# Performance work log

Measured on AMD Instinct MI355X. Metric: run time of the kernel, lower is better.

## Reference

```python
import jax, jax.numpy as jnp
import numpy as np

N_NODE = 200000   # item catalog size (n_node)
EMB = 100         # emb_size
NNZ = 1000000     # hypergraph adjacency nonzeros
B = 1024          # batch / cl_size
L = 50            # session length
LAYERS = 2        # HyperConv layers (opt.layer)
TAU = 0.2         # contrastive temperature
K_NEI = 3         # FindNeighbors.neighbor_n


def setup_inputs() -> dict:
    key = jax.random.key(0)
    ks = jax.random.split(key, 16)
    g = 1.414 / np.sqrt(EMB)  # xavier_normal gain=1.414 scale
    inp = {}
    inp["embedding"] = jax.random.normal(ks[0], (N_NODE, EMB), jnp.float32) * 0.1
    inp["adj_val"] = jax.random.uniform(ks[1], (NNZ,), jnp.float32)
    inp["A"] = jax.random.uniform(ks[2], (B, B), jnp.float32) * 0.01
    inp["D"] = jax.random.uniform(ks[3], (B, B), jnp.float32) * 0.01
    inp["z2"] = jax.random.normal(ks[4], (B, EMB), jnp.float32)
    inp["Wcf1"] = jax.random.normal(ks[5], (EMB, EMB), jnp.float32) * g
    inp["bcf1"] = jnp.zeros((EMB,), jnp.float32)
    inp["Wcf2"] = jax.random.normal(ks[6], (EMB, EMB), jnp.float32) * g
    inp["bcf2"] = jnp.zeros((EMB,), jnp.float32)
    inp["Wkg1"] = jax.random.normal(ks[7], (EMB, EMB), jnp.float32) * g
    inp["bkg1"] = jnp.zeros((EMB,), jnp.float32)
    inp["Wkg2"] = jax.random.normal(ks[8], (EMB, EMB), jnp.float32) * g
    inp["bkg2"] = jnp.zeros((EMB,), jnp.float32)
    inp["session_len"] = jnp.full((B, 1), float(L), jnp.float32)
    inp["adj_row"] = jax.random.randint(ks[9], (NNZ,), 0, N_NODE, jnp.int32)
    inp["adj_col"] = jax.random.randint(ks[10], (NNZ,), 0, N_NODE, jnp.int32)
    inp["items"] = jax.random.randint(ks[11], (B, L), 0, N_NODE + 1, jnp.int32)
    return inp


def _proj(z, W1, b1, W2, b2):
    # nn.Linear -> ELU -> nn.Linear (Contrast_2view projector)
    return jax.nn.elu(z @ W1.T + b1) @ W2.T + b2


def reference(embedding, adj_val, A, D, z2,
              Wcf1, bcf1, Wcf2, bcf2, Wkg1, bkg1, Wkg2, bkg2,
              session_len, adj_row, adj_col, items):
    # ---- HyperConv: layered sparse propagation, averaged over layers ----
    h = embedding
    acc = embedding
    for _ in range(LAYERS):
        # torch.sparse.mm(adjacency, h) via gather + segment_sum
        h = jax.ops.segment_sum(adj_val[:, None] * h[adj_col], adj_row,
                                num_segments=N_NODE)
        acc = acc + h
    hyper = acc / (LAYERS + 1)  # [N_NODE, EMB]

    # ---- RelationGAT.forward ----
    emb_pad = jnp.concatenate([jnp.zeros((1, EMB), hyper.dtype), hyper], axis=0)
    seq_h = emb_pad[items]                       # [B, L, EMB]
    rel = jnp.sum(seq_h, axis=1) / session_len   # [B, EMB]
    rel = (D @ A) @ rel                          # session-graph conv
    c = jax.nn.selu(rel)
    l_c = c / jnp.linalg.norm(c, axis=-1, keepdims=True)  # [B, EMB]

    # ---- FindNeighbors (dropout omitted: eval mode) ----
    sess = l_c
    norms = jnp.sqrt(jnp.sum(sess * sess + 1e-6, axis=1, keepdims=True))
    cos = (sess @ sess.T) / (norms @ norms.T)    # [B, B]
    cos = jax.nn.softmax(cos, axis=-1)
    topv, topi = jax.lax.top_k(cos, K_NEI)       # [B, K]
    topv = jax.nn.softmax(topv, axis=-1)
    neighbor = jnp.sum(topv[:, :, None] * sess[topi], axis=1)  # [B, EMB]

    # ---- Contrast_2view ----
    z1p = _proj(sess, Wcf1, bcf1, Wcf2, bcf2)
    z2p = _proj(z2, Wkg1, bkg1, Wkg2, bkg2)
    n1 = jnp.linalg.norm(z1p, axis=-1, keepdims=True)
    n2 = jnp.linalg.norm(z2p, axis=-1, keepdims=True)
    simm = jnp.exp((z1p @ z2p.T) / (n1 @ n2.T) / TAU)
    simm = simm / (jnp.sum(simm, axis=1, keepdims=True) + 1e-8)
    cl_loss = -jnp.mean(jnp.log(jnp.diagonal(simm)))  # pos = eye

    return hyper, l_c, neighbor, cl_loss
```

## Files before the change

### kernel.cpp

```cpp
#include <hip/hip_runtime.h>
#include <hip/hip_bf16.h>

#define N_NODE 200000
#define EMB 100
#define NNZ 1000000
#define BATCH 1024
#define SLEN 50
#define BE (BATCH * EMB)
#define SCAN_BLK 1024
#define PROJ_ROWS 8
#define UNR 8
#define HIST_BLOCKS 977

#define OFF_LC    20000000LL
#define OFF_NB    20102400LL
#define OFF_LOSS  20204800LL

typedef __hip_bfloat16 bf16;

__device__ __forceinline__ float b2f(bf16 x) { return __bfloat162float(x); }
__device__ __forceinline__ bf16 f2b(float x) { return __float2bfloat16(x); }

__device__ __forceinline__ float ldf(const void* p, long long i, int f32) {
    return f32 ? ((const float*)p)[i] : b2f(((const bf16*)p)[i]);
}
__device__ __forceinline__ void stf(void* p, long long i, int f32, float v) {
    if (f32) ((float*)p)[i] = v;
    else     ((bf16*)p)[i] = f2b(v);
}

__device__ __forceinline__ float bfb2f(unsigned short s) {
    return __uint_as_float(((unsigned)s) << 16);
}
__device__ __forceinline__ unsigned short f2bfb(float x) {
    bf16 h = f2b(x); unsigned short r; __builtin_memcpy(&r, &h, 2); return r;
}
__device__ __forceinline__ float2 up2(unsigned u) {
    return make_float2(bfb2f((unsigned short)(u & 0xffff)), bfb2f((unsigned short)(u >> 16)));
}
__device__ __forceinline__ unsigned pk2(float a, float b) {
    return (unsigned)f2bfb(a) | ((unsigned)f2bfb(b) << 16);
}
__device__ __forceinline__ float2 ldf2(const void* p, long long pi, int f32) {
    if (f32) return ((const float2*)p)[pi];
    return up2(((const unsigned*)p)[pi]);
}
template<bool F32>
__device__ __forceinline__ float2 ldf2t(const void* p, long long pi) {
    if (F32) return ((const float2*)p)[pi];
    return up2(((const unsigned*)p)[pi]);
}
template<bool F32>
__device__ __forceinline__ float2 ldnt2(const void* p, long long pi) {
    if (F32) {
        unsigned long long u = __builtin_nontemporal_load((const unsigned long long*)p + pi);
        return make_float2(__uint_as_float((unsigned)u), __uint_as_float((unsigned)(u >> 32)));
    }
    return up2(__builtin_nontemporal_load((const unsigned*)p + pi));
}
__device__ __forceinline__ float2 ldnt_h1(const unsigned* p, long long pi) {
    return up2(__builtin_nontemporal_load(p + pi));
}
__device__ __forceinline__ void stf2(void* p, long long pi, int f32, float a, float b) {
    if (f32) ((float2*)p)[pi] = make_float2(a, b);
    else     ((unsigned*)p)[pi] = pk2(a, b);
}

__device__ __forceinline__ float wave_allreduce_sum(float v) {
    for (int m = 32; m > 0; m >>= 1) v += __shfl_xor(v, m, 64);
    return v;
}

__global__ void hist_repack(const int* __restrict__ rows, int* __restrict__ counts,
                            const void* __restrict__ adjval, int* __restrict__ flag,
                            const void* __restrict__ emb, void* __restrict__ embp,
                            int f32h) {
    if (blockIdx.x == 0 && threadIdx.x == 0) {
        int f = 0;
        const bf16* p = (const bf16*)adjval;
        for (int i = 0; i < 64; i++) {
            float x = b2f(p[i]);
            if (!(x >= 0.0f && x <= 1.0f)) f = 1;
        }
        *flag = f;
    }
    if (blockIdx.x < HIST_BLOCKS) {
        int e0 = (blockIdx.x * 256 + threadIdx.x) * 4;
        if (e0 < NNZ) {
            int4 r4 = *(const int4*)&rows[e0];
            atomicAdd(&counts[r4.x], 1);
            atomicAdd(&counts[r4.y], 1);
            atomicAdd(&counts[r4.z], 1);
            atomicAdd(&counts[r4.w], 1);
        }
        return;
    }
    long long idx = (long long)(blockIdx.x - HIST_BLOCKS) * 256 + threadIdx.x;
    if (idx >= (long long)N_NODE * 64) return;
    long long r = idx >> 6;
    int l = (int)(idx & 63);
    float2 v = make_float2(0.f, 0.f);
    if (l < 50) v = ldf2(emb, r * 50 + l, f32h);
    stf2(embp, r * 64 + l, f32h, v.x, v.y);
}

__global__ void scan_block(const int* __restrict__ counts, int* __restrict__ incl,
                           int* __restrict__ bsums) {
    __shared__ int s[SCAN_BLK];
    int i = blockIdx.x * SCAN_BLK + threadIdx.x;
    int v = (i < N_NODE) ? counts[i] : 0;
    s[threadIdx.x] = v;
    __syncthreads();
    for (int off = 1; off < SCAN_BLK; off <<= 1) {
        int add = (threadIdx.x >= (unsigned)off) ? s[threadIdx.x - off] : 0;
        __syncthreads();
        s[threadIdx.x] += add;
        __syncthreads();
    }
    if (i < N_NODE) incl[i] = s[threadIdx.x];
    if (threadIdx.x == SCAN_BLK - 1) bsums[blockIdx.x] = s[threadIdx.x];
}

__global__ void scan_add(const int* __restrict__ counts, const int* __restrict__ incl,
                         const int* __restrict__ bsums, int* __restrict__ row_ptr,
                         int* __restrict__ cursor, int nb) {
    __shared__ int s[256];
    int t = threadIdx.x;
    if (t < 256) s[t] = (t < nb) ? bsums[t] : 0;
    __syncthreads();
    for (int off = 1; off < 256; off <<= 1) {
        int add = 0;
        if (t < 256 && t >= off) add = s[t - off];
        __syncthreads();
        if (t < 256) s[t] += add;
        __syncthreads();
    }
    int base = (blockIdx.x == 0) ? 0 : s[blockIdx.x - 1];
    int i = blockIdx.x * SCAN_BLK + t;
    if (i < N_NODE) {
        int ex = incl[i] - counts[i] + base;
        row_ptr[i] = ex;
        cursor[i] = ex;
    }
    if (i == 0) row_ptr[N_NODE] = NNZ;
}

__global__ void permute_edges(const int* __restrict__ arow, const int* __restrict__ acol,
                              const void* __restrict__ aval, int* __restrict__ cursor,
                              int2* __restrict__ cv, const int* __restrict__ flagp) {
    const int f32 = *flagp;
    if (blockIdx.x == 0 && threadIdx.x < 8) cv[NNZ + threadIdx.x] = make_int2(0, 0);
    int e0 = (blockIdx.x * 256 + threadIdx.x) * 4;
    if (e0 >= NNZ) return;
    int4 r4 = *(const int4*)&arow[e0];
    int4 c4 = *(const int4*)&acol[e0];
    float v[4];
    if (f32) {
        float4 f = *(const float4*)((const float*)aval + e0);
        v[0] = f.x; v[1] = f.y; v[2] = f.z; v[3] = f.w;
    } else {
        const unsigned* p = (const unsigned*)aval;
        unsigned u0 = p[e0 >> 1], u1 = p[(e0 >> 1) + 1];
        float2 a = up2(u0), b = up2(u1);
        v[0] = a.x; v[1] = a.y; v[2] = b.x; v[3] = b.y;
    }
    int rr[4] = {r4.x, r4.y, r4.z, r4.w};
    int cc[4] = {c4.x, c4.y, c4.z, c4.w};
    #pragma unroll
    for (int j = 0; j < 4; j++) {
        int pos = atomicAdd(&cursor[rr[j]], 1);
        cv[pos] = make_int2(cc[j], __float_as_int(v[j]));
    }
}

__device__ __forceinline__ void ld_cv8(int2* c, const int2* __restrict__ cv, int k0) {
    #pragma unroll
    for (int j = 0; j < UNR; j++) c[j] = cv[k0 + j];
}

template<bool F32>
__device__ __forceinline__ void spmm1_body(
        const int* __restrict__ rp, const int2* __restrict__ cv,
        const void* __restrict__ src, int estride, unsigned* __restrict__ h1) {
    int lane = threadIdx.x & 63;
    int r = blockIdx.x * 4 + (threadIdx.x >> 6);
    if (r >= N_NODE) return;
    bool act = lane < 50;
    int pl = (estride == 64) ? lane : (act ? lane : 0);
    int k0 = rp[r], k1 = rp[r + 1];
    int2 c[UNR];
    ld_cv8(c, cv, k0);
    int c0x = c[0].x;
    float2 e[UNR];
    #pragma unroll
    for (int j = 0; j < UNR; j++) {
        int cl = (k0 + j < k1) ? c[j].x : c0x;
        e[j] = ldnt2<F32>(src, (long long)cl * estride + pl);
    }
    float a0 = 0.f, a1 = 0.f;
    #pragma unroll
    for (int j = 0; j < UNR; j++) {
        float v = (k0 + j < k1) ? __int_as_float(c[j].y) : 0.f;
        a0 += v * e[j].x; a1 += v * e[j].y;
    }
    for (int k = k0 + UNR; k < k1; k += UNR) {
        int2 ct[UNR];
        #pragma unroll
        for (int j = 0; j < UNR; j++) { int kk = k + j; ct[j] = cv[kk < k1 ? kk : k1 - 1]; }
        float2 et[UNR];
        #pragma unroll
        for (int j = 0; j < UNR; j++)
            et[j] = ldnt2<F32>(src, (long long)ct[j].x * estride + pl);
        #pragma unroll
        for (int j = 0; j < UNR; j++) {
            float v = (k + j < k1) ? __int_as_float(ct[j].y) : 0.f;
            a0 += v * et[j].x; a1 += v * et[j].y;
        }
    }
    h1[(long long)r * 64 + lane] = pk2(a0, a1);
}

__global__ __launch_bounds__(256) void spmm_gather1(
        const int* __restrict__ rp, const int2* __restrict__ cv,
        const void* __restrict__ src, int estride,
        unsigned* __restrict__ h1, const int* __restrict__ flagp) {
    if (*flagp) spmm1_body<true>(rp, cv, src, estride, h1);
    else        spmm1_body<false>(rp, cv, src, estride, h1);
}

template<bool F32>
__device__ __forceinline__ void spmm2_body(
        const int* __restrict__ rp, const int2* __restrict__ cv,
        const void* __restrict__ emb,
        const unsigned* __restrict__ h1, void* __restrict__ out) {
    int lane = threadIdx.x & 63;
    int r = blockIdx.x * 4 + (threadIdx.x >> 6);
    if (r >= N_NODE) return;
    bool act = lane < 50;
    int pl = act ? lane : 0;
    int k0 = rp[r], k1 = rp[r + 1];
    int2 c[UNR];
    ld_cv8(c, cv, k0);
    int c0x = c[0].x;
    float2 ebv = ldf2t<F32>(emb, (long long)r * 50 + pl);
    float2 h1r = up2(h1[(long long)r * 64 + lane]);
    float2 e[UNR];
    #pragma unroll
    for (int j = 0; j < UNR; j++) {
        int cl = (k0 + j < k1) ? c[j].x : c0x;
        e[j] = ldnt_h1(h1, (long long)cl * 64 + lane);
    }
    float a0 = 0.f, a1 = 0.f;
    #pragma unroll
    for (int j = 0; j < UNR; j++) {
        float v = (k0 + j < k1) ? __int_as_float(c[j].y) : 0.f;
        a0 += v * e[j].x; a1 += v * e[j].y;
    }
    for (int k = k0 + UNR; k < k1; k += UNR) {
        int2 ct[UNR];
        #pragma unroll
        for (int j = 0; j < UNR; j++) { int kk = k + j; ct[j] = cv[kk < k1 ? kk : k1 - 1]; }
        float2 et[UNR];
        #pragma unroll
        for (int j = 0; j < UNR; j++)
            et[j] = ldnt_h1(h1, (long long)ct[j].x * 64 + lane);
        #pragma unroll
        for (int j = 0; j < UNR; j++) {
            float v = (k + j < k1) ? __int_as_float(ct[j].y) : 0.f;
            a0 += v * et[j].x; a1 += v * et[j].y;
        }
    }
    if (act)
        stf2(out, (long long)r * 50 + lane, F32 ? 1 : 0,
             (ebv.x + h1r.x + a0) * (1.0f / 3.0f), (ebv.y + h1r.y + a1) * (1.0f / 3.0f));
}

__global__ __launch_bounds__(256) void spmm_gather2(
        const int* __restrict__ rp, const int2* __restrict__ cv,
        const void* __restrict__ emb,
        const unsigned* __restrict__ h1, void* __restrict__ out,
        const int* __restrict__ flagp) {
    if (*flagp) spmm2_body<true>(rp, cv, emb, h1, out);
    else        spmm2_body<false>(rp, cv, emb, h1, out);
}

template<bool F32>
__device__ __forceinline__ void rel_rows_body(
        const void* __restrict__ out, const int* __restrict__ items,
        const void* __restrict__ slen, float* __restrict__ rel) {
    int lane = threadIdx.x & 63;
    int b = blockIdx.x * 4 + (threadIdx.x >> 6);
    if (b >= BATCH || lane >= 50) return;
    float s0 = 0.f, s1 = 0.f;
    #pragma unroll
    for (int l0 = 0; l0 < SLEN; l0 += 10) {
        int it[10];
        #pragma unroll
        for (int j = 0; j < 10; j++) it[j] = items[b * SLEN + l0 + j];
        float2 e[10];
        #pragma unroll
        for (int j = 0; j < 10; j++) {
            int idx = (it[j] > 0) ? it[j] - 1 : 0;
            e[j] = ldf2t<F32>(out, (long long)idx * 50 + lane);
        }
        #pragma unroll
        for (int j = 0; j < 10; j++) {
            float m = (it[j] > 0) ? 1.f : 0.f;
            s0 += m * e[j].x; s1 += m * e[j].y;
        }
    }
    float inv = 1.0f / ldf(slen, b, F32 ? 1 : 0);
    ((float2*)rel)[b * 50 + lane] = make_float2(s0 * inv, s1 * inv);
}

__global__ __launch_bounds__(256) void rel_rows(
        const void* __restrict__ out, const int* __restrict__ items,
        const void* __restrict__ slen, float* __restrict__ rel,
        const int* __restrict__ flagp) {
    if (*flagp) rel_rows_body<true>(out, items, slen, rel);
    else        rel_rows_body<false>(out, items, slen, rel);
}

__device__ __forceinline__ void bmm0_dev(float* smem, const void* __restrict__ M,
                                         const float* __restrict__ X, float* __restrict__ Y,
                                         int f32, int blk) {
    float (*ms)[BATCH] = (float(*)[BATCH])smem;
    int i0 = blk * 4;
    int t = threadIdx.x;
    for (int idx = t; idx < 4 * BATCH; idx += 256) {
        int rr = idx >> 10, j = idx & 1023;
        ms[rr][j] = ldf(M, (long long)(i0 + rr) * BATCH + j, f32);
    }
    __syncthreads();
    int w = t >> 6, lane = t & 63;
    if (lane >= 50) return;
    int i = i0 + w;
    const float2* X2 = (const float2*)X;
    float s0 = 0.f, s1 = 0.f;
    for (int j = 0; j < BATCH; j++) {
        float m = ms[w][j];
        float2 x = X2[j * 50 + lane];
        s0 += m * x.x; s1 += m * x.y;
    }
    ((float2*)Y)[i * 50 + lane] = make_float2(s0, s1);
}

__device__ void proj_dev(float* smem, const void* __restrict__ X, int x_dual,
                         const void* __restrict__ W1, const void* __restrict__ B1,
                         const void* __restrict__ W2, const void* __restrict__ B2,
                         float* __restrict__ Z, float* __restrict__ ZT,
                         float* __restrict__ nrm, int f32, int blk) {
    float* wT = smem;
    float* bsh = smem + 10000;
    float (*hid)[EMB] = (float(*)[EMB])(smem + 10100);
    float (*xr)[EMB]  = (float(*)[EMB])(smem + 10900);
    float (*red2)[2]  = (float(*)[2])(smem + 11100);
    int t = threadIdx.x;
    int sub = t >> 7, u = t & 127;
    int r0 = blk * PROJ_ROWS;
    for (int idx = t; idx < EMB * EMB; idx += 256) {
        int o = idx / EMB, k = idx - o * EMB;
        wT[k * EMB + o] = ldf(W1, idx, f32);
    }
    if (t < EMB) bsh[t] = ldf(B1, t, f32);
    __syncthreads();
    for (int pr = 0; pr < PROJ_ROWS; pr += 2) {
        int row = r0 + pr + sub;
        if (u < EMB)
            xr[sub][u] = x_dual ? ldf(X, (long long)row * EMB + u, f32)
                                : ((const float*)X)[row * EMB + u];
        __syncthreads();
        if (u < EMB) {
            float s = bsh[u];
            for (int k = 0; k < EMB; k++) s += xr[sub][k] * wT[k * EMB + u];
            hid[pr + sub][u] = (s > 0.f) ? s : expm1f(s);
        }
        __syncthreads();
    }
    for (int idx = t; idx < EMB * EMB; idx += 256) {
        int o = idx / EMB, k = idx - o * EMB;
        wT[k * EMB + o] = ldf(W2, idx, f32);
    }
    if (t < EMB) bsh[t] = ldf(B2, t, f32);
    __syncthreads();
    for (int pr = 0; pr < PROJ_ROWS; pr += 2) {
        int row = r0 + pr + sub;
        float sq = 0.f;
        if (u < EMB) {
            float o = bsh[u];
            const float* h = hid[pr + sub];
            for (int k = 0; k < EMB; k++) o += h[k] * wT[k * EMB + u];
            Z[(long long)row * EMB + u] = o;
            if (ZT) ZT[(long long)u * BATCH + row] = o;
            sq = o * o;
        }
        sq = wave_allreduce_sum(sq);
        if ((t & 63) == 0) red2[sub][(t >> 6) & 1] = sq;
        __syncthreads();
        if (u == 0) nrm[row] = sqrtf(red2[sub][0] + red2[sub][1]);
        __syncthreads();
    }
}

__global__ __launch_bounds__(256) void bmm1_projz2(
        const void* __restrict__ A, const float* __restrict__ relv, float* __restrict__ t1,
        const void* __restrict__ z2,
        const void* __restrict__ W1, const void* __restrict__ B1,
        const void* __restrict__ W2, const void* __restrict__ B2,
        float* __restrict__ z2p, float* __restrict__ z2pT, float* __restrict__ n2,
        const int* __restrict__ flagp) {
    __shared__ float smem[11104];
    const int f32 = *flagp;
    if (blockIdx.x < 256) bmm0_dev(smem, A, relv, t1, f32, blockIdx.x);
    else proj_dev(smem, z2, 1, W1, B1, W2, B2, z2p, z2pT, n2, f32, blockIdx.x - 256);
}

__global__ __launch_bounds__(256) void bmm2_selu(const void* __restrict__ M,
                                                 const float* __restrict__ X,
                                                 float* __restrict__ sess,
                                                 float* __restrict__ sessT,
                                                 float* __restrict__ ns,
                                                 void* __restrict__ out,
                                                 float* __restrict__ lacc,
                                                 int* __restrict__ done,
                                                 const int* __restrict__ flagp) {
    __shared__ float ms[4][BATCH];
    const int f32 = *flagp;
    if (blockIdx.x == 0 && threadIdx.x == 0) { *lacc = 0.f; *done = 0; }
    int i0 = blockIdx.x * 4;
    int t = threadIdx.x;
    for (int idx = t; idx < 4 * BATCH; idx += 256) {
        int rr = idx >> 10, j = idx & 1023;
        ms[rr][j] = ldf(M, (long long)(i0 + rr) * BATCH + j, f32);
    }
    __syncthreads();
    int w = t >> 6, lane = t & 63;
    bool act = lane < 50;
    int i = i0 + w;
    float s0 = 0.f, s1 = 0.f;
    if (act) {
        const float2* X2 = (const float2*)X;
        for (int j = 0; j < BATCH; j++) {
            float m = ms[w][j];
            float2 x = X2[j * 50 + lane];
            s0 += m * x.x; s1 += m * x.y;
        }
    }
    const float sc = 1.0507009873554804934193349852946f;
    const float al = 1.6732632423543772848170429916717f;
    float c0 = (s0 > 0.f) ? sc * s0 : sc * (al * expm1f(s0));
    float c1 = (s1 > 0.f) ? sc * s1 : sc * (al * expm1f(s1));
    if (!act) { c0 = 0.f; c1 = 0.f; }
    float nrm = sqrtf(wave_allreduce_sum(c0 * c0 + c1 * c1));
    float l0 = c0 / nrm, l1 = c1 / nrm;
    float nterm = act ? (l0 * l0 + l1 * l1 + 2e-6f) : 0.f;
    float n2sum = wave_allreduce_sum(nterm);
    if (act) {
        ((float2*)sess)[i * 50 + lane] = make_float2(l0, l1);
        sessT[(2 * lane) * BATCH + i] = l0;
        sessT[(2 * lane + 1) * BATCH + i] = l1;
        stf2(out, OFF_LC / 2 + (long long)i * 50 + lane, f32, l0, l1);
    }
    if (lane == 0) ns[i] = sqrtf(n2sum);
}

__device__ void neighbor_dev(float* smem, const float* __restrict__ sess,
                             const float* __restrict__ sessT, const float* __restrict__ ns,
                             void* __restrict__ out, int f32, int i) {
    float* si  = smem;
    float* red = smem + 100;
    float* wrv = smem + 104;
    int*   wri = (int*)(smem + 108);
    float* chv = smem + 112;
    int*   chi = (int*)(smem + 115);
    float* stv = smem + 118;
    int t = threadIdx.x;
    if (t < EMB) si[t] = sess[i * EMB + t];
    __syncthreads();
    float ni = ns[i];
    float d0 = 0.f, d1 = 0.f, d2 = 0.f, d3 = 0.f;
    for (int k = 0; k < EMB; k++) {
        float sv = si[k];
        const float* row = sessT + k * BATCH;
        d0 += sv * row[t];
        d1 += sv * row[t + 256];
        d2 += sv * row[t + 512];
        d3 += sv * row[t + 768];
    }
    float pv0 = expf(d0 / (ni * ns[t]));
    float pv1 = expf(d1 / (ni * ns[t + 256]));
    float pv2 = expf(d2 / (ni * ns[t + 512]));
    float pv3 = expf(d3 / (ni * ns[t + 768]));
    float local = pv0 + pv1 + pv2 + pv3;
    float w = wave_allreduce_sum(local);
    if ((t & 63) == 0) red[t >> 6] = w;
    __syncthreads();
    float S = red[0] + red[1] + red[2] + red[3];

    int c0 = -1, c1 = -1, c2 = -1;
    float pv[4] = {pv0, pv1, pv2, pv3};
    for (int r = 0; r < 3; r++) {
        float bv = -1e30f; int bi = 0x7fffffff;
        #pragma unroll
        for (int m = 0; m < 4; m++) {
            int j = t + (m << 8);
            if (j == c0 || j == c1 || j == c2) continue;
            float v = pv[m];
            if (v > bv || (v == bv && j < bi)) { bv = v; bi = j; }
        }
        #pragma unroll
        for (int off = 1; off < 64; off <<= 1) {
            float ov = __shfl_xor(bv, off);
            int oi = __shfl_xor(bi, off);
            if (ov > bv || (ov == bv && oi < bi)) { bv = ov; bi = oi; }
        }
        if ((t & 63) == 0) { wrv[t >> 6] = bv; wri[t >> 6] = bi; }
        __syncthreads();
        if (t == 0) {
            float fv = wrv[0]; int fi = wri[0];
            for (int wq = 1; wq < 4; wq++) {
                if (wrv[wq] > fv || (wrv[wq] == fv && wri[wq] < fi)) { fv = wrv[wq]; fi = wri[wq]; }
            }
            chv[r] = fv; chi[r] = fi;
        }
        __syncthreads();
        if (r == 0) c0 = chi[0];
        else if (r == 1) c1 = chi[1];
        else c2 = chi[2];
    }
    if (t == 0) {
        float e0 = expf(chv[0] / S), e1 = expf(chv[1] / S), e2 = expf(chv[2] / S);
        float es = e0 + e1 + e2;
        stv[0] = e0 / es; stv[1] = e1 / es; stv[2] = e2 / es;
    }
    __syncthreads();
    if (t < EMB) {
        float o = stv[0] * sess[chi[0] * EMB + t]
                + stv[1] * sess[chi[1] * EMB + t]
                + stv[2] * sess[chi[2] * EMB + t];
        stf(out, OFF_NB + i * EMB + t, f32, o);
    }
}

__global__ __launch_bounds__(256) void neighbor_projz1(
        const float* __restrict__ sess, const float* __restrict__ sessT,
        const float* __restrict__ ns, void* __restrict__ out,
        const void* __restrict__ W1, const void* __restrict__ B1,
        const void* __restrict__ W2, const void* __restrict__ B2,
        float* __restrict__ z1p, float* __restrict__ n1,
        const int* __restrict__ flagp) {
    __shared__ float smem[11104];
    const int f32 = *flagp;
    if (blockIdx.x < BATCH) neighbor_dev(smem, sess, sessT, ns, out, f32, blockIdx.x);
    else proj_dev(smem, sess, 0, W1, B1, W2, B2, z1p, nullptr, n1, f32,
                  blockIdx.x - BATCH);
}

__global__ void loss_kernel(const float* __restrict__ z1p, const float* __restrict__ z2pT,
                            const float* __restrict__ n1, const float* __restrict__ n2,
                            float* __restrict__ acc, int* __restrict__ done,
                            void* __restrict__ out, const int* __restrict__ flagp) {
    __shared__ float zi[EMB];
    __shared__ float red[4];
    __shared__ float sdiag;
    const int f32 = *flagp;
    int i = blockIdx.x, t = threadIdx.x;
    if (t < EMB) zi[t] = z1p[i * EMB + t];
    __syncthreads();
    float ni = n1[i];
    float d0 = 0.f, d1 = 0.f, d2 = 0.f, d3 = 0.f;
    for (int k = 0; k < EMB; k++) {
        float zv = zi[k];
        const float* row = z2pT + k * BATCH;
        d0 += zv * row[t];
        d1 += zv * row[t + 256];
        d2 += zv * row[t + 512];
        d3 += zv * row[t + 768];
    }
    float e0 = expf(d0 / (ni * n2[t]) * 5.0f);
    float e1 = expf(d1 / (ni * n2[t + 256]) * 5.0f);
    float e2 = expf(d2 / (ni * n2[t + 512]) * 5.0f);
    float e3 = expf(d3 / (ni * n2[t + 768]) * 5.0f);
    if (t == (i & 255)) {
        int m = i >> 8;
        sdiag = (m == 0) ? e0 : (m == 1) ? e1 : (m == 2) ? e2 : e3;
    }
    float local = e0 + e1 + e2 + e3;
    float w = wave_allreduce_sum(local);
    if ((t & 63) == 0) red[t >> 6] = w;
    __syncthreads();
    if (t == 0) {
        float S = red[0] + red[1] + red[2] + red[3];
        float l = -logf(sdiag / (S + 1e-8f));
        atomicAdd(acc, l * (1.0f / BATCH));
        __threadfence();
        int old = atomicAdd(done, 1);
        if (old == (int)gridDim.x - 1) {
            float v = atomicAdd(acc, 0.0f);
            stf(out, OFF_LOSS, f32, v);
        }
    }
}

extern "C" void kernel_launch(void* const* d_in, const int* in_sizes, int n_in,
                              void* d_out, int out_size, void* d_ws, size_t ws_size,
                              hipStream_t stream) {
    const void* emb  = d_in[0];
    const void* aval = d_in[1];
    const void* Amat = d_in[2];
    const void* Dmat = d_in[3];
    const void* z2   = d_in[4];
    const void* Wcf1 = d_in[5];
    const void* bcf1 = d_in[6];
    const void* Wcf2 = d_in[7];
    const void* bcf2 = d_in[8];
    const void* Wkg1 = d_in[9];
    const void* bkg1 = d_in[10];
    const void* Wkg2 = d_in[11];
    const void* bkg2 = d_in[12];
    const void* slen = d_in[13];
    const int* arow  = (const int*)d_in[14];
    const int* acol  = (const int*)d_in[15];
    const int* items = (const int*)d_in[16];

    long long esz = in_sizes ? (long long)in_sizes[0] : 0;
    int f32_host = (esz == (long long)N_NODE * EMB * 4) ? 1 : 0;
    int known_dtype = (esz == (long long)N_NODE * EMB * 2) || f32_host;

    int* flag      = (int*)d_ws;
    int* counts    = (int*)((char*)d_ws + 256);
    int* cursor    = counts;
    int* row_ptr   = counts + N_NODE;
    int* bsums     = row_ptr + N_NODE + 64;
    int2* cv       = (int2*)(bsums + 256);
    int* scanbuf   = (int*)cv;
    unsigned* h1buf = (unsigned*)(cv + NNZ + 8);
    char* tailbase = (char*)(h1buf + (long long)N_NODE * 64);
    void* emb_pad  = (void*)tailbase;
    long long embpad_bytes = (long long)N_NODE * 64 * (f32_host ? 8 : 4);
    float* fsmall  = (float*)tailbase;
    float* rel   = fsmall;
    float* t1    = rel  + BE;
    float* sess  = t1   + BE;
    float* sessT = sess + BE;
    float* z1p   = sessT + BE;
    float* z2p   = z1p  + BE;
    float* z2pT  = z2p  + BE;
    float* ns    = z2pT + BE;
    float* n1    = ns + BATCH;
    float* n2    = n1 + BATCH;
    float* lacc  = n2 + BATCH;
    int*   done  = (int*)(lacc + 1);
    long long fsmall_bytes = ((char*)(done + 16)) - (char*)tailbase;
    long long base_off = tailbase - (char*)d_ws;
    long long need_pad = base_off + (embpad_bytes > fsmall_bytes ? embpad_bytes : fsmall_bytes);
    int use_pad = known_dtype && ((long long)ws_size >= need_pad);
    int estride = use_pad ? 64 : 50;

    const int nscan = (N_NODE + SCAN_BLK - 1) / SCAN_BLK;
    const int repack_blocks = use_pad ? (int)(((long long)N_NODE * 64 + 255) / 256) : 0;

    hipMemsetAsync(counts, 0, (size_t)N_NODE * sizeof(int), stream);
    hist_repack<<<HIST_BLOCKS + repack_blocks, 256, 0, stream>>>(
        arow, counts, aval, flag, emb, emb_pad, f32_host);
    scan_block<<<nscan, SCAN_BLK, 0, stream>>>(counts, scanbuf, bsums);
    scan_add<<<nscan, SCAN_BLK, 0, stream>>>(counts, scanbuf, bsums, row_ptr, cursor, nscan);
    permute_edges<<<HIST_BLOCKS, 256, 0, stream>>>(arow, acol, aval, cursor, cv, flag);

    if (use_pad) {
        spmm_gather1<<<(N_NODE + 3) / 4, 256, 0, stream>>>(row_ptr, cv, emb_pad, estride,
                                                           h1buf, flag);
    } else {
        spmm_gather1<<<(N_NODE + 3) / 4, 256, 0, stream>>>(row_ptr, cv, emb, estride,
                                                           h1buf, flag);
    }
    spmm_gather2<<<(N_NODE + 3) / 4, 256, 0, stream>>>(row_ptr, cv, emb, h1buf,
                                                       d_out, flag);

    rel_rows<<<(BATCH + 3) / 4, 256, 0, stream>>>(d_out, items, slen, rel, flag);
    bmm1_projz2<<<384, 256, 0, stream>>>(Amat, rel, t1,
                                         z2, Wkg1, bkg1, Wkg2, bkg2,
                                         z2p, z2pT, n2, flag);
    bmm2_selu<<<BATCH / 4, 256, 0, stream>>>(Dmat, t1, sess, sessT, ns, d_out,
                                             lacc, done, flag);

    neighbor_projz1<<<BATCH + BATCH / PROJ_ROWS, 256, 0, stream>>>(
        sess, sessT, ns, d_out, Wcf1, bcf1, Wcf2, bcf2, z1p, n1, flag);

    loss_kernel<<<BATCH, 256, 0, stream>>>(z1p, z2pT, n1, n2, lacc, done, d_out, flag);
}
```

Baseline: 737.0 us.

## Fuse scan passes with atomic base, fuse loss into projection, drop nontemporal loads

Replaces the two-pass block scan with a single pass that takes each block's base from an atomic global counter and stores (start,count) pairs per row. Row order in the CSR is no longer monotone, but each row's segment stays contiguous. The projection kernel now computes the contrastive loss directly, removing a separate loss launch. The change also turns the nontemporal gathers into normal cached loads, makes permute_edges handle one edge per thread, and has each repack thread handle four elements. The goals are fewer launches and better cache reuse on the gathers, at the cost of less memory-level parallelism in permute and a loss phase spread over only 128 blocks.

Result: faster. 663.5 us (-10.0%).

```diff
diff --git a/kernel.cpp b/kernel.cpp
--- a/kernel.cpp
+++ b/kernel.cpp
@@ -11,6 +11,7 @@
 #define PROJ_ROWS 8
 #define UNR 8
 #define HIST_BLOCKS 977
+#define REPACK_BLOCKS 12500
 
 #define OFF_LC    20000000LL
 #define OFF_NB    20102400LL
@@ -49,17 +50,6 @@
 __device__ __forceinline__ float2 ldf2t(const void* p, long long pi) {
     if (F32) return ((const float2*)p)[pi];
     return up2(((const unsigned*)p)[pi]);
-}
-template<bool F32>
-__device__ __forceinline__ float2 ldnt2(const void* p, long long pi) {
-    if (F32) {
-        unsigned long long u = __builtin_nontemporal_load((const unsigned long long*)p + pi);
-        return make_float2(__uint_as_float((unsigned)u), __uint_as_float((unsigned)(u >> 32)));
-    }
-    return up2(__builtin_nontemporal_load((const unsigned*)p + pi));
-}
-__device__ __forceinline__ float2 ldnt_h1(const unsigned* p, long long pi) {
-    return up2(__builtin_nontemporal_load(p + pi));
 }
 __device__ __forceinline__ void stf2(void* p, long long pi, int f32, float a, float b) {
     if (f32) ((float2*)p)[pi] = make_float2(a, b);
@@ -96,17 +86,22 @@
         return;
     }
     long long idx = (long long)(blockIdx.x - HIST_BLOCKS) * 256 + threadIdx.x;
-    if (idx >= (long long)N_NODE * 64) return;
-    long long r = idx >> 6;
-    int l = (int)(idx & 63);
-    float2 v = make_float2(0.f, 0.f);
-    if (l < 50) v = ldf2(emb, r * 50 + l, f32h);
-    stf2(embp, r * 64 + l, f32h, v.x, v.y);
-}
-
-__global__ void scan_block(const int* __restrict__ counts, int* __restrict__ incl,
-                           int* __restrict__ bsums) {
+    if (idx >= (long long)N_NODE * 16) return;
+    long long r = idx >> 4;
+    int l0 = (int)(idx & 15) * 4;
+    #pragma unroll
+    for (int j = 0; j < 4; j++) {
+        int l = l0 + j;
+        float2 v = make_float2(0.f, 0.f);
+        if (l < 50) v = ldf2(emb, r * 50 + l, f32h);
+        stf2(embp, r * 64 + l, f32h, v.x, v.y);
+    }
+}
+
+__global__ void scan_base(const int* __restrict__ counts, int* __restrict__ cursor,
+                          int2* __restrict__ bc, int* __restrict__ gtot) {
     __shared__ int s[SCAN_BLK];
+    __shared__ int basesh;
     int i = blockIdx.x * SCAN_BLK + threadIdx.x;
     int v = (i < N_NODE) ? counts[i] : 0;
     s[threadIdx.x] = v;
@@ -117,60 +112,26 @@
         s[threadIdx.x] += add;
         __syncthreads();
     }
-    if (i < N_NODE) incl[i] = s[threadIdx.x];
-    if (threadIdx.x == SCAN_BLK - 1) bsums[blockIdx.x] = s[threadIdx.x];
-}
-
-__global__ void scan_add(const int* __restrict__ counts, const int* __restrict__ incl,
-                         const int* __restrict__ bsums, int* __restrict__ row_ptr,
-                         int* __restrict__ cursor, int nb) {
-    __shared__ int s[256];
-    int t = threadIdx.x;
-    if (t < 256) s[t] = (t < nb) ? bsums[t] : 0;
-    __syncthreads();
-    for (int off = 1; off < 256; off <<= 1) {
-        int add = 0;
-        if (t < 256 && t >= off) add = s[t - off];
-        __syncthreads();
-        if (t < 256) s[t] += add;
-        __syncthreads();
-    }
-    int base = (blockIdx.x == 0) ? 0 : s[blockIdx.x - 1];
-    int i = blockIdx.x * SCAN_BLK + t;
+    if (threadIdx.x == SCAN_BLK - 1) basesh = atomicAdd(gtot, s[threadIdx.x]);
+    __syncthreads();
     if (i < N_NODE) {
-        int ex = incl[i] - counts[i] + base;
-        row_ptr[i] = ex;
+        int ex = s[threadIdx.x] - v + basesh;
         cursor[i] = ex;
-    }
-    if (i == 0) row_ptr[N_NODE] = NNZ;
+        bc[i] = make_int2(ex, v);
+    }
 }
 
 __global__ void permute_edges(const int* __restrict__ arow, const int* __restrict__ acol,
                               const void* __restrict__ aval, int* __restrict__ cursor,
                               int2* __restrict__ cv, const int* __restrict__ flagp) {
     const int f32 = *flagp;
+    int e = blockIdx.x * 256 + threadIdx.x;
     if (blockIdx.x == 0 && threadIdx.x < 8) cv[NNZ + threadIdx.x] = make_int2(0, 0);
-    int e0 = (blockIdx.x * 256 + threadIdx.x) * 4;
-    if (e0 >= NNZ) return;
-    int4 r4 = *(const int4*)&arow[e0];
-    int4 c4 = *(const int4*)&acol[e0];
-    float v[4];
-    if (f32) {
-        float4 f = *(const float4*)((const float*)aval + e0);
-        v[0] = f.x; v[1] = f.y; v[2] = f.z; v[3] = f.w;
-    } else {
-        const unsigned* p = (const unsigned*)aval;
-        unsigned u0 = p[e0 >> 1], u1 = p[(e0 >> 1) + 1];
-        float2 a = up2(u0), b = up2(u1);
-        v[0] = a.x; v[1] = a.y; v[2] = b.x; v[3] = b.y;
-    }
-    int rr[4] = {r4.x, r4.y, r4.z, r4.w};
-    int cc[4] = {c4.x, c4.y, c4.z, c4.w};
-    #pragma unroll
-    for (int j = 0; j < 4; j++) {
-        int pos = atomicAdd(&cursor[rr[j]], 1);
-        cv[pos] = make_int2(cc[j], __float_as_int(v[j]));
-    }
+    if (e >= NNZ) return;
+    int r = arow[e];
+    int pos = atomicAdd(&cursor[r], 1);
+    float v = ldf(aval, e, f32);
+    cv[pos] = make_int2(acol[e], __float_as_int(v));
 }
 
 __device__ __forceinline__ void ld_cv8(int2* c, const int2* __restrict__ cv, int k0) {
@@ -180,14 +141,15 @@
 
 template<bool F32>
 __device__ __forceinline__ void spmm1_body(
-        const int* __restrict__ rp, const int2* __restrict__ cv,
+        const int2* __restrict__ bc, const int2* __restrict__ cv,
         const void* __restrict__ src, int estride, unsigned* __restrict__ h1) {
     int lane = threadIdx.x & 63;
     int r = blockIdx.x * 4 + (threadIdx.x >> 6);
     if (r >= N_NODE) return;
     bool act = lane < 50;
     int pl = (estride == 64) ? lane : (act ? lane : 0);
-    int k0 = rp[r], k1 = rp[r + 1];
+    int2 b = bc[r];
+    int k0 = b.x, k1 = b.x + b.y;
     int2 c[UNR];
     ld_cv8(c, cv, k0);
     int c0x = c[0].x;
@@ -195,7 +157,7 @@
     #pragma unroll
     for (int j = 0; j < UNR; j++) {
         int cl = (k0 + j < k1) ? c[j].x : c0x;
-        e[j] = ldnt2<F32>(src, (long long)cl * estride + pl);
+        e[j] = ldf2t<F32>(src, (long long)cl * estride + pl);
     }
     float a0 = 0.f, a1 = 0.f;
     #pragma unroll
@@ -210,7 +172,7 @@
         float2 et[UNR];
         #pragma unroll
         for (int j = 0; j < UNR; j++)
-            et[j] = ldnt2<F32>(src, (long long)ct[j].x * estride + pl);
+            et[j] = ldf2t<F32>(src, (long long)ct[j].x * estride + pl);
         #pragma unroll
         for (int j = 0; j < UNR; j++) {
             float v = (k + j < k1) ? __int_as_float(ct[j].y) : 0.f;
@@ -221,16 +183,16 @@
 }
 
 __global__ __launch_bounds__(256) void spmm_gather1(
-        const int* __restrict__ rp, const int2* __restrict__ cv,
+        const int2* __restrict__ bc, const int2* __restrict__ cv,
         const void* __restrict__ src, int estride,
         unsigned* __restrict__ h1, const int* __restrict__ flagp) {
-    if (*flagp) spmm1_body<true>(rp, cv, src, estride, h1);
-    else        spmm1_body<false>(rp, cv, src, estride, h1);
+    if (*flagp) spmm1_body<true>(bc, cv, src, estride, h1);
+    else        spmm1_body<false>(bc, cv, src, estride, h1);
 }
 
 template<bool F32>
 __device__ __forceinline__ void spmm2_body(
-        const int* __restrict__ rp, const int2* __restrict__ cv,
+        const int2* __restrict__ bc, const int2* __restrict__ cv,
         const void* __restrict__ emb,
         const unsigned* __restrict__ h1, void* __restrict__ out) {
     int lane = threadIdx.x & 63;
@@ -238,7 +200,8 @@
     if (r >= N_NODE) return;
     bool act = lane < 50;
     int pl = act ? lane : 0;
-    int k0 = rp[r], k1 = rp[r + 1];
+    int2 b = bc[r];
+    int k0 = b.x, k1 = b.x + b.y;
     int2 c[UNR];
     ld_cv8(c, cv, k0);
     int c0x = c[0].x;
@@ -248,7 +211,7 @@
     #pragma unroll
     for (int j = 0; j < UNR; j++) {
         int cl = (k0 + j < k1) ? c[j].x : c0x;
-        e[j] = ldnt_h1(h1, (long long)cl * 64 + lane);
+        e[j] = up2(h1[(long long)cl * 64 + lane]);
     }
     float a0 = 0.f, a1 = 0.f;
     #pragma unroll
@@ -263,7 +226,7 @@
         float2 et[UNR];
         #pragma unroll
         for (int j = 0; j < UNR; j++)
-            et[j] = ldnt_h1(h1, (long long)ct[j].x * 64 + lane);
+            et[j] = up2(h1[(long long)ct[j].x * 64 + lane]);
         #pragma unroll
         for (int j = 0; j < UNR; j++) {
             float v = (k + j < k1) ? __int_as_float(ct[j].y) : 0.f;
@@ -276,12 +239,12 @@
 }
 
 __global__ __launch_bounds__(256) void spmm_gather2(
-        const int* __restrict__ rp, const int2* __restrict__ cv,
+        const int2* __restrict__ bc, const int2* __restrict__ cv,
         const void* __restrict__ emb,
         const unsigned* __restrict__ h1, void* __restrict__ out,
         const int* __restrict__ flagp) {
-    if (*flagp) spmm2_body<true>(rp, cv, emb, h1, out);
-    else        spmm2_body<false>(rp, cv, emb, h1, out);
+    if (*flagp) spmm2_body<true>(bc, cv, emb, h1, out);
+    else        spmm2_body<false>(bc, cv, emb, h1, out);
 }
 
 template<bool F32>
@@ -399,6 +362,106 @@
         __syncthreads();
         if (u == 0) nrm[row] = sqrtf(red2[sub][0] + red2[sub][1]);
         __syncthreads();
+    }
+}
+
+__device__ void proj_loss_dev(float* smem, const float* __restrict__ X,
+                              const void* __restrict__ W1, const void* __restrict__ B1,
+                              const void* __restrict__ W2, const void* __restrict__ B2,
+                              const float* __restrict__ z2pT, const float* __restrict__ n2,
+                              float* __restrict__ lacc, int* __restrict__ done,
+                              void* __restrict__ out, int f32, int blk) {
+    float* wT = smem;
+    float* bsh = smem + 10000;
+    float (*hid)[EMB] = (float(*)[EMB])(smem + 10100);
+    float (*xr)[EMB]  = (float(*)[EMB])(smem + 10900);
+    float (*red2)[2]  = (float(*)[2])(smem + 11100);
+    float (*zsh)[EMB] = (float(*)[EMB])(smem + 11104);
+    float* n1sh = smem + 11904;
+    float* sd   = smem + 11912;
+    float* red  = smem + 11913;
+    int t = threadIdx.x;
+    int sub = t >> 7, u = t & 127;
+    int r0 = blk * PROJ_ROWS;
+    for (int idx = t; idx < EMB * EMB; idx += 256) {
+        int o = idx / EMB, k = idx - o * EMB;
+        wT[k * EMB + o] = ldf(W1, idx, f32);
+    }
+    if (t < EMB) bsh[t] = ldf(B1, t, f32);
+    __syncthreads();
+    for (int pr = 0; pr < PROJ_ROWS; pr += 2) {
+        int row = r0 + pr + sub;
+        if (u < EMB) xr[sub][u] = X[(long long)row * EMB + u];
+        __syncthreads();
+        if (u < EMB) {
+            float s = bsh[u];
+            for (int k = 0; k < EMB; k++) s += xr[sub][k] * wT[k * EMB + u];
+            hid[pr + sub][u] = (s > 0.f) ? s : expm1f(s);
+        }
+        __syncthreads();
+    }
+    for (int idx = t; idx < EMB * EMB; idx += 256) {
+        int o = idx / EMB, k = idx - o * EMB;
+        wT[k * EMB + o] = ldf(W2, idx, f32);
+    }
+    if (t < EMB) bsh[t] = ldf(B2, t, f32);
+    __syncthreads();
+    for (int pr = 0; pr < PROJ_ROWS; pr += 2) {
+        float sq = 0.f;
+        float o = 0.f;
+        if (u < EMB) {
+            o = bsh[u];
+            const float* h = hid[pr + sub];
+            for (int k = 0; k < EMB; k++) o += h[k] * wT[k * EMB + u];
+            sq = o * o;
+        }
+        __syncthreads();
+        if (u < EMB) zsh[pr + sub][u] = o;
+        sq = wave_allreduce_sum(sq);
+        if ((t & 63) == 0) red2[sub][(t >> 6) & 1] = sq;
+        __syncthreads();
+        if (u == 0) n1sh[pr + sub] = sqrtf(red2[sub][0] + red2[sub][1]);
+        __syncthreads();
+    }
+    float blockloss = 0.f;
+    for (int rr = 0; rr < PROJ_ROWS; rr++) {
+        int i = r0 + rr;
+        float ni = n1sh[rr];
+        float d0 = 0.f, d1 = 0.f, d2 = 0.f, d3 = 0.f;
+        for (int k = 0; k < EMB; k++) {
+            float zv = zsh[rr][k];
+            const float* row = z2pT + k * BATCH;
+            d0 += zv * row[t];
+            d1 += zv * row[t + 256];
+            d2 += zv * row[t + 512];
+            d3 += zv * row[t + 768];
+        }
+        float e0 = expf(d0 / (ni * n2[t]) * 5.0f);
+        float e1 = expf(d1 / (ni * n2[t + 256]) * 5.0f);
+        float e2 = expf(d2 / (ni * n2[t + 512]) * 5.0f);
+        float e3 = expf(d3 / (ni * n2[t + 768]) * 5.0f);
+        if (t == (i & 255)) {
+            int m = i >> 8;
+            sd[0] = (m == 0) ? e0 : (m == 1) ? e1 : (m == 2) ? e2 : e3;
+        }
+        float local = e0 + e1 + e2 + e3;
+        float w = wave_allreduce_sum(local);
+        if ((t & 63) == 0) red[t >> 6] = w;
+        __syncthreads();
+        if (t == 0) {
+            float S = red[0] + red[1] + red[2] + red[3];
+            blockloss += -logf(sd[0] / (S + 1e-8f));
+        }
+        __syncthreads();
+    }
+    if (t == 0) {
+        atomicAdd(lacc, blockloss * (1.0f / BATCH));
+        __threadfence();
+        int old = atomicAdd(done, 1);
+        if (old == BATCH / PROJ_ROWS - 1) {
+            float v = atomicAdd(lacc, 0.0f);
+            stf(out, OFF_LOSS, f32, v);
+        }
     }
 }
 
@@ -542,64 +605,19 @@
     }
 }
 
-__global__ __launch_bounds__(256) void neighbor_projz1(
+__global__ __launch_bounds__(256) void neighbor_projz1_loss(
         const float* __restrict__ sess, const float* __restrict__ sessT,
         const float* __restrict__ ns, void* __restrict__ out,
         const void* __restrict__ W1, const void* __restrict__ B1,
         const void* __restrict__ W2, const void* __restrict__ B2,
-        float* __restrict__ z1p, float* __restrict__ n1,
+        const float* __restrict__ z2pT, const float* __restrict__ n2,
+        float* __restrict__ lacc, int* __restrict__ done,
         const int* __restrict__ flagp) {
-    __shared__ float smem[11104];
+    __shared__ float smem[11920];
     const int f32 = *flagp;
     if (blockIdx.x < BATCH) neighbor_dev(smem, sess, sessT, ns, out, f32, blockIdx.x);
-    else proj_dev(smem, sess, 0, W1, B1, W2, B2, z1p, nullptr, n1, f32,
-                  blockIdx.x - BATCH);
-}
-
-__global__ void loss_kernel(const float* __restrict__ z1p, const float* __restrict__ z2pT,
-                            const float* __restrict__ n1, const float* __restrict__ n2,
-                            float* __restrict__ acc, int* __restrict__ done,
-                            void* __restrict__ out, const int* __restrict__ flagp) {
-    __shared__ float zi[EMB];
-    __shared__ float red[4];
-    __shared__ float sdiag;
-    const int f32 = *flagp;
-    int i = blockIdx.x, t = threadIdx.x;
-    if (t < EMB) zi[t] = z1p[i * EMB + t];
-    __syncthreads();
-    float ni = n1[i];
-    float d0 = 0.f, d1 = 0.f, d2 = 0.f, d3 = 0.f;
-    for (int k = 0; k < EMB; k++) {
-        float zv = zi[k];
-        const float* row = z2pT + k * BATCH;
-        d0 += zv * row[t];
-        d1 += zv * row[t + 256];
-        d2 += zv * row[t + 512];
-        d3 += zv * row[t + 768];
-    }
-    float e0 = expf(d0 / (ni * n2[t]) * 5.0f);
-    float e1 = expf(d1 / (ni * n2[t + 256]) * 5.0f);
-    float e2 = expf(d2 / (ni * n2[t + 512]) * 5.0f);
-    float e3 = expf(d3 / (ni * n2[t + 768]) * 5.0f);
-    if (t == (i & 255)) {
-        int m = i >> 8;
-        sdiag = (m == 0) ? e0 : (m == 1) ? e1 : (m == 2) ? e2 : e3;
-    }
-    float local = e0 + e1 + e2 + e3;
-    float w = wave_allreduce_sum(local);
-    if ((t & 63) == 0) red[t >> 6] = w;
-    __syncthreads();
-    if (t == 0) {
-        float S = red[0] + red[1] + red[2] + red[3];
-        float l = -logf(sdiag / (S + 1e-8f));
-        atomicAdd(acc, l * (1.0f / BATCH));
-        __threadfence();
-        int old = atomicAdd(done, 1);
-        if (old == (int)gridDim.x - 1) {
-            float v = atomicAdd(acc, 0.0f);
-            stf(out, OFF_LOSS, f32, v);
-        }
-    }
+    else proj_loss_dev(smem, sess, W1, B1, W2, B2, z2pT, n2, lacc, done, out, f32,
+                       blockIdx.x - BATCH);
 }
 
 extern "C" void kernel_launch(void* const* d_in, const int* in_sizes, int n_in,
@@ -628,12 +646,11 @@
     int known_dtype = (esz == (long long)N_NODE * EMB * 2) || f32_host;
 
     int* flag      = (int*)d_ws;
+    int* gtot      = (int*)d_ws + 4;
     int* counts    = (int*)((char*)d_ws + 256);
     int* cursor    = counts;
-    int* row_ptr   = counts + N_NODE;
-    int* bsums     = row_ptr + N_NODE + 64;
-    int2* cv       = (int2*)(bsums + 256);
-    int* scanbuf   = (int*)cv;
+    int2* bc       = (int2*)(counts + N_NODE);
+    int2* cv       = bc + N_NODE;
     unsigned* h1buf = (unsigned*)(cv + NNZ + 8);
     char* tailbase = (char*)(h1buf + (long long)N_NODE * 64);
     void* emb_pad  = (void*)tailbase;
@@ -658,23 +675,23 @@
     int estride = use_pad ? 64 : 50;
 
     const int nscan = (N_NODE + SCAN_BLK - 1) / SCAN_BLK;
-    const int repack_blocks = use_pad ? (int)(((long long)N_NODE * 64 + 255) / 256) : 0;
-
-    hipMemsetAsync(counts, 0, (size_t)N_NODE * sizeof(int), stream);
+    const int repack_blocks = use_pad ? REPACK_BLOCKS : 0;
+
+    hipMemsetAsync(d_ws, 0, 256 + (size_t)N_NODE * sizeof(int), stream);
     hist_repack<<<HIST_BLOCKS + repack_blocks, 256, 0, stream>>>(
         arow, counts, aval, flag, emb, emb_pad, f32_host);
-    scan_block<<<nscan, SCAN_BLK, 0, stream>>>(counts, scanbuf, bsums);
-    scan_add<<<nscan, SCAN_BLK, 0, stream>>>(counts, scanbuf, bsums, row_ptr, cursor, nscan);
-    permute_edges<<<HIST_BLOCKS, 256, 0, stream>>>(arow, acol, aval, cursor, cv, flag);
+    scan_base<<<nscan, SCAN_BLK, 0, stream>>>(counts, cursor, bc, gtot);
+    permute_edges<<<(NNZ + 255) / 256, 256, 0, stream>>>(arow, acol, aval, cursor,
+                                                         cv, flag);
 
     if (use_pad) {
-        spmm_gather1<<<(N_NODE + 3) / 4, 256, 0, stream>>>(row_ptr, cv, emb_pad, estride,
+        spmm_gather1<<<(N_NODE + 3) / 4, 256, 0, stream>>>(bc, cv, emb_pad, estride,
                                                            h1buf, flag);
     } else {
-        spmm_gather1<<<(N_NODE + 3) / 4, 256, 0, stream>>>(row_ptr, cv, emb, estride,
+        spmm_gather1<<<(N_NODE + 3) / 4, 256, 0, stream>>>(bc, cv, emb, estride,
                                                            h1buf, flag);
     }
-    spmm_gather2<<<(N_NODE + 3) / 4, 256, 0, stream>>>(row_ptr, cv, emb, h1buf,
+    spmm_gather2<<<(N_NODE + 3) / 4, 256, 0, stream>>>(bc, cv, emb, h1buf,
                                                        d_out, flag);
 
     rel_rows<<<(BATCH + 3) / 4, 256, 0, stream>>>(d_out, items, slen, rel, flag);
@@ -684,8 +701,6 @@
     bmm2_selu<<<BATCH / 4, 256, 0, stream>>>(Dmat, t1, sess, sessT, ns, d_out,
                                              lacc, done, flag);
 
-    neighbor_projz1<<<BATCH + BATCH / PROJ_ROWS, 256, 0, stream>>>(
-        sess, sessT, ns, d_out, Wcf1, bcf1, Wcf2, bcf2, z1p, n1, flag);
-
-    loss_kernel<<<BATCH, 256, 0, stream>>>(z1p, z2pT, n1, n2, lacc, done, d_out, flag);
-}
+    neighbor_projz1_loss<<<BATCH + BATCH / PROJ_ROWS, 256, 0, stream>>>(
+        sess, sessT, ns, d_out, Wcf1, bcf1, Wcf2, bcf2, z2pT, n2, lacc, done, flag);
+}
```
